# Performance work log

Hardware: AMD Instinct MI355X
Metric: run time of the kernel (lower is better)

The kernel has to match this reference:

```python
import jax, jax.numpy as jnp
import numpy as np

N = 4096        # nodes
E = 131072      # edges (avg degree 32)
IN_F = 256      # in_features
OUT_F = 64      # out_features per head
H = 8           # num_heads


def setup_inputs() -> dict:
    key = jax.random.key(0)
    k1, k2, k3, k4 = jax.random.split(key, 4)
    x = jax.random.normal(k1, (N, IN_F), dtype=jnp.float32)
    # xavier-ish scales for the learned params
    W = jax.random.normal(k2, (IN_F, OUT_F * H), dtype=jnp.float32) * 0.06
    a = jax.random.normal(k3, (2 * OUT_F, 1), dtype=jnp.float32) * 0.12
    edge_index = jax.random.randint(k4, (2, E), 0, N, dtype=jnp.int32)
    return {"x": x, "W": W, "a": a, "edge_index": edge_index}


def reference(x, W, a, edge_index):
    n = x.shape[0]
    Wh = (x @ W).reshape(n, H, OUT_F)          # [N, H, F]
    src, dst = edge_index[0], edge_index[1]
    # edge score: cat(Wh[src], Wh[dst]) @ a == Wh[src]@a1 + Wh[dst]@a2
    a1 = a[:OUT_F, 0]                           # [F]
    a2 = a[OUT_F:2 * OUT_F, 0]                  # [F]
    alpha_src = Wh @ a1                         # [N, H]
    alpha_dst = Wh @ a2                         # [N, H]
    edge_e = jax.nn.leaky_relu(alpha_src[src] + alpha_dst[dst], 0.2)  # [E, H]
    # dense scatter exactly as the original module (non-edges stay 0 in softmax)
    attention = jnp.zeros((n, n, H), dtype=x.dtype).at[src, dst].set(edge_e)
    attention = jax.nn.softmax(attention, axis=1)
    # dropout is identity in eval mode
    h_prime = jnp.einsum('nmh,mhf->nhf', attention, Wh)  # [N, H, F]
    return h_prime.reshape(n, H * OUT_F)        # concat=True
```

## Files before the change

### kernel.cpp

```cpp
#include <hip/hip_runtime.h>
#include <hip/hip_bf16.h>

constexpr int NN    = 4096;
constexpr int EE    = 131072;
constexpr int IN_F  = 256;
constexpr int OUT_F = 64;
constexpr int HH    = 8;
constexpr int HF    = OUT_F * HH;
constexpr int CAP   = 128;

typedef __attribute__((ext_vector_type(8))) short bf16x8;
typedef __attribute__((ext_vector_type(4))) float f32x4;

__device__ __forceinline__ unsigned short f2b(float f) {
    unsigned int u = __float_as_uint(f);
    u = u + 0x7FFFu + ((u >> 16) & 1u);
    return (unsigned short)(u >> 16);
}
__device__ __forceinline__ float b2f(unsigned int lo16) {
    return __uint_as_float(lo16 << 16);
}

__global__ __launch_bounds__(256) void preconvert(const float* __restrict__ x,
                                                  const float* __restrict__ W,
                                                  unsigned short* __restrict__ xhi,
                                                  unsigned short* __restrict__ xlo,
                                                  unsigned short* __restrict__ WThi,
                                                  unsigned short* __restrict__ WTlo,
                                                  float* __restrict__ S,
                                                  int* __restrict__ cnt) {
    int b = blockIdx.x, t = threadIdx.x;
    if (b < 512) {
        int base = (b * 256 + t) * 8;
        float4 v0 = *(const float4*)(x + base);
        float4 v1 = *(const float4*)(x + base + 4);
        float f[8] = {v0.x, v0.y, v0.z, v0.w, v1.x, v1.y, v1.z, v1.w};
        unsigned short hi[8], lo[8];
#pragma unroll
        for (int j = 0; j < 8; ++j) {
            hi[j] = f2b(f[j]);
            lo[j] = f2b(f[j] - b2f(hi[j]));
        }
        *(ushort4*)(xhi + base)     = make_ushort4(hi[0], hi[1], hi[2], hi[3]);
        *(ushort4*)(xhi + base + 4) = make_ushort4(hi[4], hi[5], hi[6], hi[7]);
        *(ushort4*)(xlo + base)     = make_ushort4(lo[0], lo[1], lo[2], lo[3]);
        *(ushort4*)(xlo + base + 4) = make_ushort4(lo[4], lo[5], lo[6], lo[7]);
    } else {
        int bb = b - 512;
        int gt2 = bb * 256 + t;
        if (gt2 < NN) cnt[gt2] = 0;
        else if (gt2 < NN + HF) S[gt2 - NN] = 0.f;
        int n  = bb * 8 + (t >> 5);
        int kb = (t & 31) * 8;
        unsigned short hi[8], lo[8];
#pragma unroll
        for (int j = 0; j < 8; ++j) {
            float f = W[(size_t)(kb + j) * HF + n];
            hi[j] = f2b(f);
            lo[j] = f2b(f - b2f(hi[j]));
        }
        size_t o = (size_t)n * 256 + kb;
        *(ushort4*)(WThi + o)     = make_ushort4(hi[0], hi[1], hi[2], hi[3]);
        *(ushort4*)(WThi + o + 4) = make_ushort4(hi[4], hi[5], hi[6], hi[7]);
        *(ushort4*)(WTlo + o)     = make_ushort4(lo[0], lo[1], lo[2], lo[3]);
        *(ushort4*)(WTlo + o + 4) = make_ushort4(lo[4], lo[5], lo[6], lo[7]);
    }
}

__global__ __launch_bounds__(256) void gemm_mfma(const unsigned short* __restrict__ xhi,
                                                 const unsigned short* __restrict__ xlo,
                                                 const unsigned short* __restrict__ WThi,
                                                 const unsigned short* __restrict__ WTlo,
                                                 const float* __restrict__ a,
                                                 const int* __restrict__ src,
                                                 const int* __restrict__ dst,
                                                 int* __restrict__ cnt,
                                                 int* __restrict__ csr_dst,
                                                 unsigned short* __restrict__ Whb,
                                                 float* __restrict__ asrc,
                                                 float* __restrict__ adst,
                                                 float* __restrict__ S) {
    __shared__ unsigned short Bhi_s[64][264];
    __shared__ unsigned short Blo_s[64][264];
    __shared__ float Scol[64];
    int b = blockIdx.x;
    int t = threadIdx.x;

    {
        int e = b * 256 + t;
        int s = src[e], d = dst[e];
        int pos = atomicAdd(&cnt[s], 1);
        csr_dst[(s << 7) + pos] = d;
    }

    int m0 = (b >> 3) * 64;
    int n0 = (b & 7) * 64;
    if (t < 64) Scol[t] = 0.f;

#pragma unroll
    for (int it = 0; it < 8; ++it) {
        int flat = it * 256 + t;
        int row  = flat >> 5;
        int cu   = flat & 31;
        *(uint4*)(&Bhi_s[row][cu * 8]) =
            *(const uint4*)(WThi + (size_t)(n0 + row) * 256 + cu * 8);
        *(uint4*)(&Blo_s[row][cu * 8]) =
            *(const uint4*)(WTlo + (size_t)(n0 + row) * 256 + cu * 8);
    }
    __syncthreads();

    int w  = t >> 6;
    int l  = t & 63;
    int kg = l >> 4;
    int ln = l & 15;
    int arow = m0 + w * 16 + ln;

    f32x4 acc[4] = {};

#pragma unroll
    for (int ks = 0; ks < 8; ++ks) {
        size_t aoff = (size_t)arow * 256 + ks * 32 + kg * 8;
        bf16x8 ahi = *(const bf16x8*)(xhi + aoff);
        bf16x8 alo = *(const bf16x8*)(xlo + aoff);
#pragma unroll
        for (int nt = 0; nt < 4; ++nt) {
            const unsigned short* bp = &Bhi_s[nt * 16 + ln][ks * 32 + kg * 8];
            const unsigned short* lp = &Blo_s[nt * 16 + ln][ks * 32 + kg * 8];
            bf16x8 bhi = *(const bf16x8*)bp;
            bf16x8 blo = *(const bf16x8*)lp;
            acc[nt] = __builtin_amdgcn_mfma_f32_16x16x32_bf16(ahi, bhi, acc[nt], 0, 0, 0);
            acc[nt] = __builtin_amdgcn_mfma_f32_16x16x32_bf16(ahi, blo, acc[nt], 0, 0, 0);
            acc[nt] = __builtin_amdgcn_mfma_f32_16x16x32_bf16(alo, bhi, acc[nt], 0, 0, 0);
        }
    }

#pragma unroll
    for (int nt = 0; nt < 4; ++nt)
#pragma unroll
        for (int i = 0; i < 4; ++i) {
            int row = m0 + w * 16 + kg * 4 + i;
            Whb[(size_t)row * HF + n0 + nt * 16 + ln] = f2b(acc[nt][i]);
        }

    int h = n0 >> 6;
    float a1v[4], a2v[4];
#pragma unroll
    for (int nt = 0; nt < 4; ++nt) {
        a1v[nt] = a[nt * 16 + ln];
        a2v[nt] = a[OUT_F + nt * 16 + ln];
    }
#pragma unroll
    for (int i = 0; i < 4; ++i) {
        float p1 = acc[0][i] * a1v[0] + acc[1][i] * a1v[1] +
                   acc[2][i] * a1v[2] + acc[3][i] * a1v[3];
        float p2 = acc[0][i] * a2v[0] + acc[1][i] * a2v[1] +
                   acc[2][i] * a2v[2] + acc[3][i] * a2v[3];
#pragma unroll
        for (int mask = 1; mask < 16; mask <<= 1) {
            p1 += __shfl_xor(p1, mask);
            p2 += __shfl_xor(p2, mask);
        }
        if (ln == 0) {
            int node = m0 + w * 16 + kg * 4 + i;
            asrc[node * HH + h] = p1;
            adst[node * HH + h] = p2;
        }
    }

#pragma unroll
    for (int nt = 0; nt < 4; ++nt) {
        float cs = acc[nt][0] + acc[nt][1] + acc[nt][2] + acc[nt][3];
        cs += __shfl_xor(cs, 16);
        cs += __shfl_xor(cs, 32);
        if (kg == 0) atomicAdd(&Scol[nt * 16 + ln], cs);
    }
    __syncthreads();
    if (t < 64) atomicAdd(&S[n0 + t], Scol[t]);
}

__global__ __launch_bounds__(512) void aggregate_kernel(const unsigned short* __restrict__ Whb,
                                                        const float* __restrict__ asrc,
                                                        const float* __restrict__ adst,
                                                        const float* __restrict__ S,
                                                        const int* __restrict__ cnt,
                                                        const int* __restrict__ csr_dst,
                                                        float* __restrict__ out) {
    __shared__ int           midx[CAP];
    __shared__ unsigned char dupf[CAP];
    __shared__ float         wbuf[CAP * HH];
    __shared__ float         as_sh[HH];
    __shared__ float         denom[HH];
    __shared__ float         red[8][HF];
    int i = blockIdx.x;
    int t = threadIdx.x;
    int deg = cnt[i];
    if (deg > CAP) deg = CAP;

    if (t < HH) as_sh[t] = asrc[i * HH + t];
    for (int j = t; j < deg; j += 512) midx[j] = csr_dst[(i << 7) + j];
    __syncthreads();

    for (int j = t; j < deg; j += 512) {
        int m = midx[j];
        unsigned char f = 0;
        for (int k = 0; k < j; ++k)
            if (midx[k] == m) { f = 1; break; }
        dupf[j] = f;
    }
    __syncthreads();

    for (int idx = t; idx < deg * HH; idx += 512) {
        int sl = idx >> 3, h = idx & 7;
        float w = 0.f;
        if (!dupf[sl]) {
            float xv = as_sh[h] + adst[midx[sl] * HH + h];
            xv = (xv > 0.f) ? xv : 0.2f * xv;
            w = __expf(xv) - 1.f;
        }
        wbuf[idx] = w;
    }
    __syncthreads();

    if (t < 128) {
        int h = t >> 4, ln = t & 15;
        float p = 0.f;
        for (int sl = ln; sl < deg; sl += 16) p += wbuf[sl * HH + h];
#pragma unroll
        for (int mask = 1; mask < 16; mask <<= 1) p += __shfl_xor(p, mask);
        if (ln == 0) denom[h] = (float)NN + p;
    }
    __syncthreads();

    int g = t >> 6;
    int r = t & 63;
    int h = r >> 3;
    float accv[8] = {};

    int j = g;
    uint4 uC = {0, 0, 0, 0};
    float wC = 0.f;
    if (j < deg) {
        wC = wbuf[j * HH + h];
        uC = *(const uint4*)(Whb + ((size_t)midx[j] << 9) + (r << 3));
    }
    while (j < deg) {
        int jn = j + 8;
        uint4 uN = {0, 0, 0, 0};
        float wN = 0.f;
        if (jn < deg) {
            wN = wbuf[jn * HH + h];
            uN = *(const uint4*)(Whb + ((size_t)midx[jn] << 9) + (r << 3));
        }
        accv[0] += wC * b2f(uC.x & 0xFFFFu);
        accv[1] += wC * b2f(uC.x >> 16);
        accv[2] += wC * b2f(uC.y & 0xFFFFu);
        accv[3] += wC * b2f(uC.y >> 16);
        accv[4] += wC * b2f(uC.z & 0xFFFFu);
        accv[5] += wC * b2f(uC.z >> 16);
        accv[6] += wC * b2f(uC.w & 0xFFFFu);
        accv[7] += wC * b2f(uC.w >> 16);
        uC = uN; wC = wN; j = jn;
    }

    float4 v0 = {accv[0], accv[1], accv[2], accv[3]};
    float4 v1 = {accv[4], accv[5], accv[6], accv[7]};
    *(float4*)(&red[g][r * 8])     = v0;
    *(float4*)(&red[g][r * 8 + 4]) = v1;
    __syncthreads();

    float tot = S[t];
#pragma unroll
    for (int gg = 0; gg < 8; ++gg) tot += red[gg][t];
    out[((size_t)i << 9) + t] = tot / denom[t >> 6];
}

extern "C" void kernel_launch(void* const* d_in, const int* in_sizes, int n_in,
                              void* d_out, int out_size, void* d_ws, size_t ws_size,
                              hipStream_t stream) {
    const float* x  = (const float*)d_in[0];
    const float* W  = (const float*)d_in[1];
    const float* a  = (const float*)d_in[2];
    const int*   ei = (const int*)d_in[3];
    const int* src = ei;
    const int* dst = ei + EE;
    float* out = (float*)d_out;

    char* ws = (char*)d_ws;
    unsigned short* Whb  = (unsigned short*)(ws + 0);
    unsigned short* xhi  = (unsigned short*)(ws + 4194304);
    unsigned short* xlo  = (unsigned short*)(ws + 6291456);
    unsigned short* WThi = (unsigned short*)(ws + 8388608);
    unsigned short* WTlo = (unsigned short*)(ws + 8650752);
    float* asrc     = (float*)(ws + 8912896);
    float* adst     = (float*)(ws + 9043968);
    int*   csr_dst  = (int*)  (ws + 9175040);
    float* S        = (float*)(ws + 11272192);
    int*   cnt      = (int*)  (ws + 11274240);

    preconvert<<<576, 256, 0, stream>>>(x, W, xhi, xlo, WThi, WTlo, S, cnt);

    gemm_mfma<<<512, 256, 0, stream>>>(xhi, xlo, WThi, WTlo, a, src, dst,
                                       cnt, csr_dst, Whb, asrc, adst, S);

    aggregate_kernel<<<NN, 512, 0, stream>>>(Whb, asrc, adst, S, cnt, csr_dst, out);
}
```

Measured before the change: 119.1 us.

## Fuse x bf16 split into GEMM and deepen aggregate gather prefetch

Removes the separate pass that splits x into hi/lo bf16 buffers in global memory. The GEMM now reads fp32 x directly and does the split in registers, which saves an intermediate write and read and shrinks the prep kernel to handle only W and the zero-init. The aggregate kernel's gather loop now prefetches two rows ahead instead of one, to hide more of the latency of the scattered Whb loads. In exchange, each GEMM block redoes the x conversion for every output column tile (8 tiles), and register pressure rises in both kernels.

Result: no change. 118.3 us (-0.7%).

```diff
diff --git a/kernel.cpp b/kernel.cpp
--- a/kernel.cpp
+++ b/kernel.cpp
@@ -21,36 +21,14 @@
     return __uint_as_float(lo16 << 16);
 }
 
-__global__ __launch_bounds__(256) void preconvert(const float* __restrict__ x,
-                                                  const float* __restrict__ W,
-                                                  unsigned short* __restrict__ xhi,
-                                                  unsigned short* __restrict__ xlo,
-                                                  unsigned short* __restrict__ WThi,
-                                                  unsigned short* __restrict__ WTlo,
-                                                  float* __restrict__ S,
-                                                  int* __restrict__ cnt) {
+__global__ __launch_bounds__(256) void prep(const float* __restrict__ W,
+                                            unsigned short* __restrict__ WThi,
+                                            unsigned short* __restrict__ WTlo,
+                                            float* __restrict__ S,
+                                            int* __restrict__ cnt) {
     int b = blockIdx.x, t = threadIdx.x;
-    if (b < 512) {
-        int base = (b * 256 + t) * 8;
-        float4 v0 = *(const float4*)(x + base);
-        float4 v1 = *(const float4*)(x + base + 4);
-        float f[8] = {v0.x, v0.y, v0.z, v0.w, v1.x, v1.y, v1.z, v1.w};
-        unsigned short hi[8], lo[8];
-#pragma unroll
-        for (int j = 0; j < 8; ++j) {
-            hi[j] = f2b(f[j]);
-            lo[j] = f2b(f[j] - b2f(hi[j]));
-        }
-        *(ushort4*)(xhi + base)     = make_ushort4(hi[0], hi[1], hi[2], hi[3]);
-        *(ushort4*)(xhi + base + 4) = make_ushort4(hi[4], hi[5], hi[6], hi[7]);
-        *(ushort4*)(xlo + base)     = make_ushort4(lo[0], lo[1], lo[2], lo[3]);
-        *(ushort4*)(xlo + base + 4) = make_ushort4(lo[4], lo[5], lo[6], lo[7]);
-    } else {
-        int bb = b - 512;
-        int gt2 = bb * 256 + t;
-        if (gt2 < NN) cnt[gt2] = 0;
-        else if (gt2 < NN + HF) S[gt2 - NN] = 0.f;
-        int n  = bb * 8 + (t >> 5);
+    if (b < 64) {
+        int n  = b * 8 + (t >> 5);
         int kb = (t & 31) * 8;
         unsigned short hi[8], lo[8];
 #pragma unroll
@@ -64,11 +42,14 @@
         *(ushort4*)(WThi + o + 4) = make_ushort4(hi[4], hi[5], hi[6], hi[7]);
         *(ushort4*)(WTlo + o)     = make_ushort4(lo[0], lo[1], lo[2], lo[3]);
         *(ushort4*)(WTlo + o + 4) = make_ushort4(lo[4], lo[5], lo[6], lo[7]);
-    }
-}
-
-__global__ __launch_bounds__(256) void gemm_mfma(const unsigned short* __restrict__ xhi,
-                                                 const unsigned short* __restrict__ xlo,
+    } else {
+        int gt = (b - 64) * 256 + t;
+        if (gt < NN) cnt[gt] = 0;
+        else if (gt < NN + HF) S[gt - NN] = 0.f;
+    }
+}
+
+__global__ __launch_bounds__(256) void gemm_mfma(const float* __restrict__ xf,
                                                  const unsigned short* __restrict__ WThi,
                                                  const unsigned short* __restrict__ WTlo,
                                                  const float* __restrict__ a,
@@ -120,14 +101,20 @@
 #pragma unroll
     for (int ks = 0; ks < 8; ++ks) {
         size_t aoff = (size_t)arow * 256 + ks * 32 + kg * 8;
-        bf16x8 ahi = *(const bf16x8*)(xhi + aoff);
-        bf16x8 alo = *(const bf16x8*)(xlo + aoff);
+        float4 v0 = *(const float4*)(xf + aoff);
+        float4 v1 = *(const float4*)(xf + aoff + 4);
+        float fv[8] = {v0.x, v0.y, v0.z, v0.w, v1.x, v1.y, v1.z, v1.w};
+        bf16x8 ahi, alo;
+#pragma unroll
+        for (int j = 0; j < 8; ++j) {
+            unsigned short hi = f2b(fv[j]);
+            ahi[j] = (short)hi;
+            alo[j] = (short)f2b(fv[j] - b2f(hi));
+        }
 #pragma unroll
         for (int nt = 0; nt < 4; ++nt) {
-            const unsigned short* bp = &Bhi_s[nt * 16 + ln][ks * 32 + kg * 8];
-            const unsigned short* lp = &Blo_s[nt * 16 + ln][ks * 32 + kg * 8];
-            bf16x8 bhi = *(const bf16x8*)bp;
-            bf16x8 blo = *(const bf16x8*)lp;
+            bf16x8 bhi = *(const bf16x8*)(&Bhi_s[nt * 16 + ln][ks * 32 + kg * 8]);
+            bf16x8 blo = *(const bf16x8*)(&Blo_s[nt * 16 + ln][ks * 32 + kg * 8]);
             acc[nt] = __builtin_amdgcn_mfma_f32_16x16x32_bf16(ahi, bhi, acc[nt], 0, 0, 0);
             acc[nt] = __builtin_amdgcn_mfma_f32_16x16x32_bf16(ahi, blo, acc[nt], 0, 0, 0);
             acc[nt] = __builtin_amdgcn_mfma_f32_16x16x32_bf16(alo, bhi, acc[nt], 0, 0, 0);
@@ -236,30 +223,37 @@
     int h = r >> 3;
     float accv[8] = {};
 
-    int j = g;
-    uint4 uC = {0, 0, 0, 0};
-    float wC = 0.f;
-    if (j < deg) {
-        wC = wbuf[j * HH + h];
-        uC = *(const uint4*)(Whb + ((size_t)midx[j] << 9) + (r << 3));
-    }
+    int j0 = g, j1 = g + 8;
+    uint4 u0 = {0, 0, 0, 0}, u1 = {0, 0, 0, 0};
+    float w0 = 0.f, w1 = 0.f;
+    if (j0 < deg) {
+        w0 = wbuf[j0 * HH + h];
+        u0 = *(const uint4*)(Whb + ((size_t)midx[j0] << 9) + (r << 3));
+    }
+    if (j1 < deg) {
+        w1 = wbuf[j1 * HH + h];
+        u1 = *(const uint4*)(Whb + ((size_t)midx[j1] << 9) + (r << 3));
+    }
+    int j = j0;
     while (j < deg) {
-        int jn = j + 8;
-        uint4 uN = {0, 0, 0, 0};
-        float wN = 0.f;
+        int jn = j + 16;
+        uint4 un = {0, 0, 0, 0};
+        float wn = 0.f;
         if (jn < deg) {
-            wN = wbuf[jn * HH + h];
-            uN = *(const uint4*)(Whb + ((size_t)midx[jn] << 9) + (r << 3));
-        }
-        accv[0] += wC * b2f(uC.x & 0xFFFFu);
-        accv[1] += wC * b2f(uC.x >> 16);
-        accv[2] += wC * b2f(uC.y & 0xFFFFu);
-        accv[3] += wC * b2f(uC.y >> 16);
-        accv[4] += wC * b2f(uC.z & 0xFFFFu);
-        accv[5] += wC * b2f(uC.z >> 16);
-        accv[6] += wC * b2f(uC.w & 0xFFFFu);
-        accv[7] += wC * b2f(uC.w >> 16);
-        uC = uN; wC = wN; j = jn;
+            wn = wbuf[jn * HH + h];
+            un = *(const uint4*)(Whb + ((size_t)midx[jn] << 9) + (r << 3));
+        }
+        accv[0] += w0 * b2f(u0.x & 0xFFFFu);
+        accv[1] += w0 * b2f(u0.x >> 16);
+        accv[2] += w0 * b2f(u0.y & 0xFFFFu);
+        accv[3] += w0 * b2f(u0.y >> 16);
+        accv[4] += w0 * b2f(u0.z & 0xFFFFu);
+        accv[5] += w0 * b2f(u0.z >> 16);
+        accv[6] += w0 * b2f(u0.w & 0xFFFFu);
+        accv[7] += w0 * b2f(u0.w >> 16);
+        u0 = u1; w0 = w1;
+        u1 = un; w1 = wn;
+        j += 8;
     }
 
     float4 v0 = {accv[0], accv[1], accv[2], accv[3]};
@@ -287,19 +281,17 @@
 
     char* ws = (char*)d_ws;
     unsigned short* Whb  = (unsigned short*)(ws + 0);
-    unsigned short* xhi  = (unsigned short*)(ws + 4194304);
-    unsigned short* xlo  = (unsigned short*)(ws + 6291456);
-    unsigned short* WThi = (unsigned short*)(ws + 8388608);
-    unsigned short* WTlo = (unsigned short*)(ws + 8650752);
-    float* asrc     = (float*)(ws + 8912896);
-    float* adst     = (float*)(ws + 9043968);
-    int*   csr_dst  = (int*)  (ws + 9175040);
-    float* S        = (float*)(ws + 11272192);
-    int*   cnt      = (int*)  (ws + 11274240);
-
-    preconvert<<<576, 256, 0, stream>>>(x, W, xhi, xlo, WThi, WTlo, S, cnt);
-
-    gemm_mfma<<<512, 256, 0, stream>>>(xhi, xlo, WThi, WTlo, a, src, dst,
+    unsigned short* WThi = (unsigned short*)(ws + 4194304);
+    unsigned short* WTlo = (unsigned short*)(ws + 4456448);
+    float* asrc     = (float*)(ws + 4718592);
+    float* adst     = (float*)(ws + 4849664);
+    int*   csr_dst  = (int*)  (ws + 4980736);
+    float* S        = (float*)(ws + 7077888);
+    int*   cnt      = (int*)  (ws + 7079936);
+
+    prep<<<82, 256, 0, stream>>>(W, WThi, WTlo, S, cnt);
+
+    gemm_mfma<<<512, 256, 0, stream>>>(x, WThi, WTlo, a, src, dst,
                                        cnt, csr_dst, Whb, asrc, adst, S);
 
     aggregate_kernel<<<NN, 512, 0, stream>>>(Whb, asrc, adst, S, cnt, csr_dst, out);
```
